# Kernel optimization log

Measured on AMD Instinct MI355X. Metric: run time of the kernel, lower is better.

Reference implementation:

```python
import jax, jax.numpy as jnp
import numpy as np

N_NODES = 50000
IN_DIM = 128
HID = 2 * IN_DIM  # 256, per module: hidden_dim = input_dims * 2
FC1 = 1024
FC2 = 512
N_ACT = 64
N_EDGES = 800000
N_AGENTS = 16384


def _layernorm(h, g, b, eps=1e-5):
    mu = jnp.mean(h, axis=-1, keepdims=True)
    var = jnp.var(h, axis=-1, keepdims=True)
    return (h - mu) * jax.lax.rsqrt(var + eps) * g + b


def setup_inputs() -> dict:
    key = jax.random.key(0)
    ks = jax.random.split(key, 16)
    def u(k, shape, fan_in):
        s = 1.0 / np.sqrt(fan_in)
        return jax.random.uniform(k, shape, jnp.float32, -s, s)
    inp = {}
    inp["x"] = jax.random.normal(ks[0], (N_NODES, IN_DIM), jnp.float32)
    inp["action"] = jax.random.normal(ks[1], (N_AGENTS, N_ACT), jnp.float32)
    inp["edge_index"] = jax.random.randint(ks[2], (2, N_EDGES), 0, N_NODES, jnp.int32)
    inp["agent_idx"] = jax.random.randint(ks[3], (N_AGENTS,), 0, N_NODES, jnp.int32)
    # GCNConv params (linear no bias + separate bias)
    inp["W_gcn"] = u(ks[4], (IN_DIM, HID), IN_DIM)
    inp["b_gcn"] = jnp.zeros((HID,), jnp.float32)
    # fc1, fc2 (custom uniform init per module)
    inp["W1"] = u(ks[5], (HID, FC1), FC1)
    inp["b1"] = u(ks[6], (FC1,), FC1)
    inp["g1"] = jnp.ones((FC1,), jnp.float32)
    inp["beta1"] = jnp.zeros((FC1,), jnp.float32)
    inp["W2"] = u(ks[7], (FC1, FC2), FC2)
    inp["b2"] = u(ks[8], (FC2,), FC2)
    inp["g2"] = jnp.ones((FC2,), jnp.float32)
    inp["beta2"] = jnp.zeros((FC2,), jnp.float32)
    inp["Wa"] = u(ks[9], (N_ACT, FC2), FC2)
    inp["ba"] = u(ks[10], (FC2,), FC2)
    inp["Wq"] = jax.random.uniform(ks[11], (FC2, 1), jnp.float32, -0.003, 0.003)
    inp["bq"] = jax.random.uniform(ks[12], (1,), jnp.float32, -0.003, 0.003)
    return inp


def reference(x, action, W_gcn, b_gcn, W1, b1, g1, beta1, W2, b2, g2, beta2, Wa, ba, Wq, bq, edge_index, agent_idx):
    N = x.shape[0]
    # GCNConv: add self-loops, symmetric D^-1/2 (A+I) D^-1/2 normalization
    loops = jnp.arange(N, dtype=edge_index.dtype)
    src = jnp.concatenate([edge_index[0], loops])
    dst = jnp.concatenate([edge_index[1], loops])
    h = x @ W_gcn  # [N, HID] transform before aggregation
    deg = jax.ops.segment_sum(jnp.ones_like(dst, dtype=h.dtype), dst, num_segments=N)
    dinv = jax.lax.rsqrt(jnp.maximum(deg, 1.0))  # deg >= 1 due to self-loops
    norm = dinv[src] * dinv[dst]  # [E+N]
    agg = jax.ops.segment_sum(h[src] * norm[:, None], dst, num_segments=N) + b_gcn
    # masked gather of agent nodes, then critic MLP
    z = jax.nn.relu(agg[agent_idx])  # [A, HID]
    s = jax.nn.relu(_layernorm(z @ W1 + b1, g1, beta1))
    s = _layernorm(s @ W2 + b2, g2, beta2)
    a = action @ Wa + ba
    sa = jax.nn.relu(s + a)
    return sa @ Wq + bq  # [A, 1]
```

## Files before the change

kernel.cpp:

```cpp
#include <hip/hip_runtime.h>
#include <hip/hip_bf16.h>

typedef _Float16 f16;
typedef _Float16 __attribute__((ext_vector_type(8))) half8;
typedef _Float16 __attribute__((ext_vector_type(4))) half4;
typedef float __attribute__((ext_vector_type(4))) floatx4;

#define IN_DIM 128
#define HID    256
#define FC1    1024
#define FC2    512
#define NACT   64
#define BUCKET 128

__device__ __forceinline__ void transpose_tile(const float* __restrict__ in, f16* __restrict__ out,
                                               int K, int N, int bx, int by, int tid) {
    __shared__ f16 tile[32][33];
    int k0 = bx * 32, n0 = by * 32;
    int tx = tid & 31, ty = tid >> 5;
    #pragma unroll
    for (int i = 0; i < 4; ++i)
        tile[ty + i * 8][tx] = (f16)in[(size_t)(k0 + ty + i * 8) * N + n0 + tx];
    __syncthreads();
    #pragma unroll
    for (int i = 0; i < 4; ++i)
        out[(size_t)(n0 + ty + i * 8) * K + k0 + tx] = tile[tx][ty + i * 8];
}

__device__ __forceinline__ void cvt8(const float* __restrict__ in, f16* __restrict__ out, long gi) {
    float4 a = *(const float4*)&in[gi * 8];
    float4 b = *(const float4*)&in[gi * 8 + 4];
    half8 pk;
    pk[0] = (f16)a.x; pk[1] = (f16)a.y; pk[2] = (f16)a.z; pk[3] = (f16)a.w;
    pk[4] = (f16)b.x; pk[5] = (f16)b.y; pk[6] = (f16)b.z; pk[7] = (f16)b.w;
    *(half8*)&out[gi * 8] = pk;
}

__global__ __launch_bounds__(256)
void prep_kernel(const float* __restrict__ Wgcn, const float* __restrict__ W1,
                 const float* __restrict__ W2, const float* __restrict__ Wa,
                 const float* __restrict__ action, const float* __restrict__ x,
                 f16* WgcnT, f16* W1T, f16* W2T, f16* WaT, f16* act16, f16* x16,
                 int* degcnt, int* needed, int* n_needed, int* cursor, int N, int A) {
    int b = blockIdx.x, tid = threadIdx.x;
    if (b < 196) {
        int i = b * 256 + tid;
        if (i < N) { degcnt[i] = 0; needed[i] = 0; }
        if (b == 0 && tid == 0) *n_needed = 0;
        return;
    }
    b -= 196;
    if (b < 64)  { cursor[b * 256 + tid] = 0; return; }
    b -= 64;
    if (b < 32)  { transpose_tile(Wgcn, WgcnT, IN_DIM, HID, b & 3, b >> 2, tid); return; }
    b -= 32;
    if (b < 256) { transpose_tile(W1, W1T, HID, FC1, b & 7, b >> 3, tid); return; }
    b -= 256;
    if (b < 512) { transpose_tile(W2, W2T, FC1, FC2, b & 31, b >> 5, tid); return; }
    b -= 512;
    if (b < 32)  { transpose_tile(Wa, WaT, NACT, FC2, b & 1, b >> 1, tid); return; }
    b -= 32;
    if (b < 512) { cvt8(action, act16, (long)b * 256 + tid); return; }
    b -= 512;
    cvt8(x, x16, (long)b * 256 + tid);
}

__global__ void markdeg_kernel(const int* __restrict__ agent_idx, const int* __restrict__ edst,
                               int* __restrict__ needed, int* __restrict__ needed_list,
                               int* __restrict__ n_needed, int* __restrict__ degcnt, int A, int E) {
    int b = blockIdx.x;
    if (b < 64) {
        int i = b * 256 + threadIdx.x;
        if (i < A) {
            int idx = agent_idx[i];
            if (atomicCAS(&needed[idx], 0, -1) == 0) {
                int p = atomicAdd(n_needed, 1);
                needed_list[p] = idx;
                needed[idx] = p + 1;
            }
        }
        return;
    }
    int e = (b - 64) * 256 + threadIdx.x;
    if (e < E) atomicAdd(&degcnt[edst[e]], 1);
}

__global__ void dssfill_kernel(const int* __restrict__ degcnt, const int* __restrict__ needed,
                               const int* __restrict__ agent_idx, float* __restrict__ dinv,
                               int* __restrict__ agent_slot,
                               const int* __restrict__ esrc, const int* __restrict__ edst,
                               int* __restrict__ cursor, int* __restrict__ srcbuf,
                               int N, int A, int E) {
    int b = blockIdx.x;
    int tid = threadIdx.x;
    if (b < 196) {
        int i = b * 256 + tid;
        if (i < N) dinv[i] = rsqrtf((float)degcnt[i] + 1.0f);
        return;
    }
    b -= 196;
    if (b < 64) {
        int i = b * 256 + tid;
        if (i < A) agent_slot[i] = needed[agent_idx[i]] - 1;
        return;
    }
    b -= 64;
    int e = b * 256 + tid;
    if (e < E) {
        int d = edst[e];
        int s = needed[d];
        if (s != 0) {
            int slot = s - 1;
            int pos = atomicAdd(&cursor[slot], 1);
            if (pos < BUCKET) srcbuf[slot * BUCKET + pos] = esrc[e];
        }
    }
}

__global__ __launch_bounds__(256)
void gather_x_kernel(const int* __restrict__ needed_list, const int* __restrict__ n_needed,
                     const int* __restrict__ degcnt,
                     const int* __restrict__ srcbuf, const float* __restrict__ dinv,
                     const f16* __restrict__ x16, f16* __restrict__ xagg) {
    int w = (blockIdx.x * 256 + threadIdx.x) >> 6;
    int lane = threadIdx.x & 63;
    if (w >= *n_needed) return;
    int d = needed_list[w];
    float dd = dinv[d];
    int beg = w * BUCKET;
    int cnt = degcnt[d];
    if (cnt > BUCKET) cnt = BUCKET;
    union { unsigned u; f16 h[2]; } ld0, ld1, ld2, ld3;
    ld0.u = *(const unsigned*)&x16[(size_t)d * IN_DIM + lane * 2];
    float ax = (float)ld0.h[0] * dd * dd, ay = (float)ld0.h[1] * dd * dd;
    int j = 0;
    for (; j + 3 < cnt; j += 4) {
        int s0 = srcbuf[beg + j], s1 = srcbuf[beg + j + 1];
        int s2 = srcbuf[beg + j + 2], s3 = srcbuf[beg + j + 3];
        float n0 = dinv[s0] * dd, n1 = dinv[s1] * dd;
        float n2 = dinv[s2] * dd, n3 = dinv[s3] * dd;
        ld0.u = *(const unsigned*)&x16[(size_t)s0 * IN_DIM + lane * 2];
        ld1.u = *(const unsigned*)&x16[(size_t)s1 * IN_DIM + lane * 2];
        ld2.u = *(const unsigned*)&x16[(size_t)s2 * IN_DIM + lane * 2];
        ld3.u = *(const unsigned*)&x16[(size_t)s3 * IN_DIM + lane * 2];
        ax = fmaf((float)ld0.h[0], n0, ax); ay = fmaf((float)ld0.h[1], n0, ay);
        ax = fmaf((float)ld1.h[0], n1, ax); ay = fmaf((float)ld1.h[1], n1, ay);
        ax = fmaf((float)ld2.h[0], n2, ax); ay = fmaf((float)ld2.h[1], n2, ay);
        ax = fmaf((float)ld3.h[0], n3, ax); ay = fmaf((float)ld3.h[1], n3, ay);
    }
    for (; j < cnt; ++j) {
        int s0 = srcbuf[beg + j];
        float n0 = dinv[s0] * dd;
        ld0.u = *(const unsigned*)&x16[(size_t)s0 * IN_DIM + lane * 2];
        ax = fmaf((float)ld0.h[0], n0, ax);
        ay = fmaf((float)ld0.h[1], n0, ay);
    }
    union { f16 h[2]; unsigned u; } pk;
    pk.h[0] = (f16)ax; pk.h[1] = (f16)ay;
    *(unsigned*)&xagg[(size_t)w * IN_DIM + lane * 2] = pk.u;
}

__device__ __forceinline__ void swz_decode(int bid, int log2ny, int& bx, int& by) {
    int xcd = bid & 7;
    int pos = bid >> 3;
    bx = (pos >> log2ny) * 8 + xcd;
    by = pos & ((1 << log2ny) - 1);
}

template<bool RELU, bool LIMIT>
__device__ __forceinline__ void gemm_tile64(f16* __restrict__ smA, f16* __restrict__ smB,
                                            const f16* __restrict__ A, const f16* __restrict__ BT,
                                            f16* __restrict__ C, const float* __restrict__ bias,
                                            const int* __restrict__ limit,
                                            int bx, int by, int N, int K) {
    if (LIMIT && bx * 64 >= *limit) return;
    const int tid = threadIdx.x;
    const int lane = tid & 63;
    const int wave = tid >> 6;
    const int wr = wave >> 1, wc = wave & 1;
    const long bm = (long)bx * 64, bn = (long)by * 64;

    size_t aoff[2], boff[2];
    #pragma unroll
    for (int t = 0; t < 2; ++t) {
        int ci = t * 256 + tid;
        int r = ci >> 3, s = ci & 7, ks = s ^ (r & 7);
        aoff[t] = (size_t)(bm + r) * K + ks * 8;
        boff[t] = (size_t)(bn + r) * K + ks * 8;
    }
    int aidx[2][2], bidx[2][2];
    const int kc = lane >> 4;
    #pragma unroll
    for (int kk = 0; kk < 2; ++kk) {
        #pragma unroll
        for (int i = 0; i < 2; ++i) {
            int ar = wr * 32 + i * 16 + (lane & 15);
            aidx[kk][i] = ar * 64 + ((kk * 4 + kc) ^ (ar & 7)) * 8;
            int br = wc * 32 + i * 16 + (lane & 15);
            bidx[kk][i] = br * 64 + ((kk * 4 + kc) ^ (br & 7)) * 8;
        }
    }

    const int NT = K >> 6;
    auto stage = [&](int buf, int k0) {
        #pragma unroll
        for (int t = 0; t < 2; ++t) {
            __builtin_amdgcn_global_load_lds(
                (const __attribute__((address_space(1))) void*)(A + aoff[t] + k0),
                (__attribute__((address_space(3))) void*)(&smA[buf * 4096 + (t * 256 + tid) * 8]), 16, 0, 0);
            __builtin_amdgcn_global_load_lds(
                (const __attribute__((address_space(1))) void*)(BT + boff[t] + k0),
                (__attribute__((address_space(3))) void*)(&smB[buf * 4096 + (t * 256 + tid) * 8]), 16, 0, 0);
        }
    };

    floatx4 acc[2][2] = {};
    stage(0, 0);
    asm volatile("s_waitcnt vmcnt(0)" ::: "memory");
    __builtin_amdgcn_s_barrier();
    int cur = 0;
    for (int t = 0; t < NT; ++t) {
        if (t + 1 < NT) stage(cur ^ 1, (t + 1) << 6);
        #pragma unroll
        for (int kk = 0; kk < 2; ++kk) {
            half8 af[2], bf[2];
            #pragma unroll
            for (int i = 0; i < 2; ++i) {
                af[i] = *(const half8*)&smA[cur * 4096 + aidx[kk][i]];
                bf[i] = *(const half8*)&smB[cur * 4096 + bidx[kk][i]];
            }
            #pragma unroll
            for (int mi = 0; mi < 2; ++mi)
                #pragma unroll
                for (int ni = 0; ni < 2; ++ni)
                    acc[mi][ni] = __builtin_amdgcn_mfma_f32_16x16x32_f16(af[mi], bf[ni], acc[mi][ni], 0, 0, 0);
        }
        asm volatile("s_waitcnt vmcnt(0)" ::: "memory");
        __builtin_amdgcn_s_barrier();
        cur ^= 1;
    }
    const int col0 = (int)bn + wc * 32 + (lane & 15);
    const int row0 = (int)bm + wr * 32 + (lane >> 4) * 4;
    #pragma unroll
    for (int ni = 0; ni < 2; ++ni) {
        int col = col0 + ni * 16;
        float bz = bias[col];
        #pragma unroll
        for (int mi = 0; mi < 2; ++mi) {
            #pragma unroll
            for (int q = 0; q < 4; ++q) {
                int row = row0 + mi * 16 + q;
                float v = acc[mi][ni][q] + bz;
                if (RELU) v = fmaxf(v, 0.f);
                C[(size_t)row * N + col] = (f16)v;
            }
        }
    }
}

template<bool RELU, bool LIMIT>
__global__ __launch_bounds__(256)
void gemm64_kernel(const f16* __restrict__ A, const f16* __restrict__ BT,
                   f16* __restrict__ C, const float* __restrict__ bias,
                   const int* __restrict__ limit, int N, int K, int log2ny) {
    __shared__ __align__(16) f16 smA[2 * 4096];
    __shared__ __align__(16) f16 smB[2 * 4096];
    int bx, by;
    swz_decode(blockIdx.x, log2ny, bx, by);
    gemm_tile64<RELU, LIMIT>(smA, smB, A, BT, C, bias, limit, bx, by, N, K);
}

template<bool LIMIT>
__device__ __forceinline__ void gemm_tile128(f16* __restrict__ smA, f16* __restrict__ smB,
                                             const f16* __restrict__ A, const f16* __restrict__ BT,
                                             f16* __restrict__ C, const float* __restrict__ bias,
                                             const int* __restrict__ limit,
                                             int bx, int by, int N, int K) {
    if (LIMIT && bx * 128 >= *limit) return;
    const int tid = threadIdx.x;
    const int lane = tid & 63;
    const int wave = tid >> 6;
    const int wr = wave >> 1, wc = wave & 1;
    const long bm = (long)bx * 128, bn = (long)by * 128;

    size_t aoff[4], boff[4];
    #pragma unroll
    for (int t = 0; t < 4; ++t) {
        int ci = t * 256 + tid;
        int r = ci >> 3, s = ci & 7, ks = s ^ (r & 7);
        aoff[t] = (size_t)(bm + r) * K + ks * 8;
        boff[t] = (size_t)(bn + r) * K + ks * 8;
    }
    int aidx[2][4], bidx[2][4];
    const int kc = lane >> 4;
    #pragma unroll
    for (int kk = 0; kk < 2; ++kk) {
        #pragma unroll
        for (int i = 0; i < 4; ++i) {
            int ar = wr * 64 + i * 16 + (lane & 15);
            aidx[kk][i] = ar * 64 + ((kk * 4 + kc) ^ (ar & 7)) * 8;
            int br = wc * 64 + i * 16 + (lane & 15);
            bidx[kk][i] = br * 64 + ((kk * 4 + kc) ^ (br & 7)) * 8;
        }
    }

    const int NT = K >> 6;
    auto stage = [&](int buf, int k0) {
        #pragma unroll
        for (int t = 0; t < 4; ++t) {
            __builtin_amdgcn_global_load_lds(
                (const __attribute__((address_space(1))) void*)(A + aoff[t] + k0),
                (__attribute__((address_space(3))) void*)(&smA[buf * 8192 + (t * 256 + tid) * 8]), 16, 0, 0);
            __builtin_amdgcn_global_load_lds(
                (const __attribute__((address_space(1))) void*)(BT + boff[t] + k0),
                (__attribute__((address_space(3))) void*)(&smB[buf * 8192 + (t * 256 + tid) * 8]), 16, 0, 0);
        }
    };

    floatx4 acc[4][4] = {};
    stage(0, 0);
    asm volatile("s_waitcnt vmcnt(0)" ::: "memory");
    __builtin_amdgcn_s_barrier();
    int cur = 0;
    for (int t = 0; t < NT; ++t) {
        if (t + 1 < NT) stage(cur ^ 1, (t + 1) << 6);
        #pragma unroll
        for (int kk = 0; kk < 2; ++kk) {
            half8 af[4], bf[4];
            #pragma unroll
            for (int i = 0; i < 4; ++i) {
                af[i] = *(const half8*)&smA[cur * 8192 + aidx[kk][i]];
                bf[i] = *(const half8*)&smB[cur * 8192 + bidx[kk][i]];
            }
            #pragma unroll
            for (int mi = 0; mi < 4; ++mi)
                #pragma unroll
                for (int ni = 0; ni < 4; ++ni)
                    acc[mi][ni] = __builtin_amdgcn_mfma_f32_16x16x32_f16(af[mi], bf[ni], acc[mi][ni], 0, 0, 0);
        }
        asm volatile("s_waitcnt vmcnt(0)" ::: "memory");
        __builtin_amdgcn_s_barrier();
        cur ^= 1;
    }
    const int col0 = (int)bn + wc * 64 + (lane & 15);
    const int row0 = (int)bm + wr * 64 + (lane >> 4) * 4;
    #pragma unroll
    for (int ni = 0; ni < 4; ++ni) {
        int col = col0 + ni * 16;
        float bz = bias[col];
        #pragma unroll
        for (int mi = 0; mi < 4; ++mi) {
            #pragma unroll
            for (int q = 0; q < 4; ++q) {
                int row = row0 + mi * 16 + q;
                C[(size_t)row * N + col] = (f16)(acc[mi][ni][q] + bz);
            }
        }
    }
}

template<bool LIMIT>
__global__ __launch_bounds__(256)
void gemm128_kernel(const f16* __restrict__ A, const f16* __restrict__ BT,
                    f16* __restrict__ C, const float* __restrict__ bias,
                    const int* __restrict__ limit, int N, int K, int log2ny) {
    __shared__ __align__(16) f16 smA[2 * 8192];
    __shared__ __align__(16) f16 smB[2 * 8192];
    int bx, by;
    swz_decode(blockIdx.x, log2ny, bx, by);
    gemm_tile128<LIMIT>(smA, smB, A, BT, C, bias, limit, bx, by, N, K);
}

__global__ __launch_bounds__(256)
void gemm_dual_kernel(const f16* __restrict__ A0, const f16* __restrict__ BT0, f16* __restrict__ C0,
                      const float* __restrict__ bias0, const int* __restrict__ limit, int K0,
                      const f16* __restrict__ A1, const f16* __restrict__ BT1, f16* __restrict__ C1,
                      const float* __restrict__ bias1, int K1, int half, int N) {
    __shared__ __align__(16) f16 smA[2 * 8192];
    __shared__ __align__(16) f16 smB[2 * 8192];
    int bid = blockIdx.x;
    int bx, by;
    if (bid < half) {
        swz_decode(bid, 2, bx, by);
        gemm_tile128<true>(smA, smB, A0, BT0, C0, bias0, limit, bx, by, N, K0);
    } else {
        swz_decode(bid - half, 2, bx, by);
        gemm_tile128<false>(smA, smB, A1, BT1, C1, bias1, nullptr, bx, by, N, K1);
    }
}

__global__ __launch_bounds__(256)
void ln_relu_f16_kernel(f16* __restrict__ s, const float* __restrict__ g,
                        const float* __restrict__ b, const int* __restrict__ nn) {
    int row = blockIdx.x;
    if (row >= *nn) return;
    f16* p = s + (size_t)row * FC1;
    int tid = threadIdx.x;
    half4 v = *(const half4*)&p[tid * 4];
    float f0 = (float)v[0], f1 = (float)v[1], f2 = (float)v[2], f3 = (float)v[3];
    float sum = f0 + f1 + f2 + f3;
    float sq = f0 * f0 + f1 * f1 + f2 * f2 + f3 * f3;
    #pragma unroll
    for (int off = 32; off > 0; off >>= 1) {
        sum += __shfl_down(sum, off);
        sq  += __shfl_down(sq, off);
    }
    __shared__ float ssum[4], ssq[4];
    int wid = tid >> 6;
    if ((tid & 63) == 0) { ssum[wid] = sum; ssq[wid] = sq; }
    __syncthreads();
    float tot = ssum[0] + ssum[1] + ssum[2] + ssum[3];
    float tq  = ssq[0] + ssq[1] + ssq[2] + ssq[3];
    float mu = tot * (1.0f / FC1);
    float var = tq * (1.0f / FC1) - mu * mu;
    float rs = rsqrtf(var + 1e-5f);
    float4 gg = *(const float4*)&g[tid * 4];
    float4 bb = *(const float4*)&b[tid * 4];
    half4 o;
    o[0] = (f16)fmaxf((f0 - mu) * rs * gg.x + bb.x, 0.f);
    o[1] = (f16)fmaxf((f1 - mu) * rs * gg.y + bb.y, 0.f);
    o[2] = (f16)fmaxf((f2 - mu) * rs * gg.z + bb.z, 0.f);
    o[3] = (f16)fmaxf((f3 - mu) * rs * gg.w + bb.w, 0.f);
    *(half4*)&p[tid * 4] = o;
}

__global__ __launch_bounds__(256)
void final_f16_kernel(const f16* __restrict__ s2, const f16* __restrict__ ab,
                      const int* __restrict__ agent_slot,
                      const float* __restrict__ g2, const float* __restrict__ b2,
                      const float* __restrict__ Wq, const float* __restrict__ bq,
                      float* __restrict__ out) {
    int row = blockIdx.x;
    int slot = agent_slot[row];
    const f16* p = s2 + (size_t)slot * FC2;
    int tid = threadIdx.x;
    float v0 = (float)p[tid * 2], v1 = (float)p[tid * 2 + 1];
    float sum = v0 + v1;
    float sq = v0 * v0 + v1 * v1;
    #pragma unroll
    for (int off = 32; off > 0; off >>= 1) {
        sum += __shfl_down(sum, off);
        sq  += __shfl_down(sq, off);
    }
    __shared__ float ssum[4], ssq[4], spart[4];
    int wid = tid >> 6;
    if ((tid & 63) == 0) { ssum[wid] = sum; ssq[wid] = sq; }
    __syncthreads();
    float tot = ssum[0] + ssum[1] + ssum[2] + ssum[3];
    float tq  = ssq[0] + ssq[1] + ssq[2] + ssq[3];
    float mu = tot * (1.0f / FC2);
    float var = tq * (1.0f / FC2) - mu * mu;
    float rs = rsqrtf(var + 1e-5f);
    float a0 = (float)ab[(size_t)row * FC2 + tid * 2];
    float a1 = (float)ab[(size_t)row * FC2 + tid * 2 + 1];
    float g0 = g2[tid * 2], g1 = g2[tid * 2 + 1];
    float bb0 = b2[tid * 2], bb1 = b2[tid * 2 + 1];
    float sa0 = fmaxf((v0 - mu) * rs * g0 + bb0 + a0, 0.f);
    float sa1 = fmaxf((v1 - mu) * rs * g1 + bb1 + a1, 0.f);
    float part = sa0 * Wq[tid * 2] + sa1 * Wq[tid * 2 + 1];
    #pragma unroll
    for (int off = 32; off > 0; off >>= 1) part += __shfl_down(part, off);
    if ((tid & 63) == 0) spart[wid] = part;
    __syncthreads();
    if (tid == 0) out[row] = spart[0] + spart[1] + spart[2] + spart[3] + bq[0];
}

extern "C" void kernel_launch(void* const* d_in, const int* in_sizes, int n_in,
                              void* d_out, int out_size, void* d_ws, size_t ws_size,
                              hipStream_t stream) {
    const float* x        = (const float*)d_in[0];
    const float* action   = (const float*)d_in[1];
    const int*   edge     = (const int*)d_in[2];
    const int*   agent_idx= (const int*)d_in[3];
    const float* W_gcn    = (const float*)d_in[4];
    const float* b_gcn    = (const float*)d_in[5];
    const float* W1       = (const float*)d_in[6];
    const float* b1       = (const float*)d_in[7];
    const float* g1       = (const float*)d_in[8];
    const float* beta1    = (const float*)d_in[9];
    const float* W2       = (const float*)d_in[10];
    const float* b2       = (const float*)d_in[11];
    const float* g2       = (const float*)d_in[12];
    const float* beta2    = (const float*)d_in[13];
    const float* Wa       = (const float*)d_in[14];
    const float* ba       = (const float*)d_in[15];
    const float* Wq       = (const float*)d_in[16];
    const float* bq       = (const float*)d_in[17];
    float* out = (float*)d_out;

    const int N = in_sizes[0] / IN_DIM;
    const int E = in_sizes[2] / 2;
    const int A = in_sizes[3];
    const int* esrc = edge;
    const int* edst = edge + E;

    char* ws = (char*)d_ws;
    size_t off = 0;
    auto carve = [&](size_t bytes) -> char* {
        char* p = ws + off;
        off += (bytes + 255) & ~(size_t)255;
        return p;
    };
    int*   degcnt     = (int*)  carve((size_t)N * 4);
    int*   needed     = (int*)  carve((size_t)N * 4);
    float* dinv       = (float*)carve((size_t)N * 4);
    int*   cursor     = (int*)  carve((size_t)A * 4);
    int*   needed_list= (int*)  carve((size_t)A * 4);
    int*   n_needed   = (int*)  carve(256);
    int*   agent_slot = (int*)  carve((size_t)A * 4);
    int*   srcbuf     = (int*)  carve((size_t)A * BUCKET * 4);
    f16*   WgcnT      = (f16*)  carve((size_t)HID * IN_DIM * 2);
    f16*   W1T        = (f16*)  carve((size_t)FC1 * HID * 2);
    f16*   W2T        = (f16*)  carve((size_t)FC2 * FC1 * 2);
    f16*   WaT        = (f16*)  carve((size_t)FC2 * NACT * 2);
    f16*   act16      = (f16*)  carve((size_t)A * NACT * 2);
    f16*   x16        = (f16*)  carve((size_t)N * IN_DIM * 2);
    f16*   xagg       = (f16*)  carve((size_t)A * IN_DIM * 2);
    f16*   z          = (f16*)  carve((size_t)A * HID * 2);
    f16*   s1         = (f16*)  carve((size_t)A * FC1 * 2);
    f16*   s2         = (f16*)  carve((size_t)A * FC2 * 2);
    f16*   abuf       = (f16*)  carve((size_t)A * FC2 * 2);
    (void)ws_size;

    const int eblk = (E + 255) / 256;

    prep_kernel<<<196 + 64 + 32 + 256 + 512 + 32 + 512 + eblk, 256, 0, stream>>>(
        W_gcn, W1, W2, Wa, action, x, WgcnT, W1T, W2T, WaT, act16, x16,
        degcnt, needed, n_needed, cursor, N, A);
    markdeg_kernel<<<64 + eblk, 256, 0, stream>>>(agent_idx, edst, needed, needed_list,
                                                  n_needed, degcnt, A, E);
    dssfill_kernel<<<196 + 64 + eblk, 256, 0, stream>>>(degcnt, needed, agent_idx, dinv,
                                                        agent_slot, esrc, edst, cursor,
                                                        srcbuf, N, A, E);
    gather_x_kernel<<<(A + 3) / 4, 256, 0, stream>>>(needed_list, n_needed, degcnt,
                                                     srcbuf, dinv, x16, xagg);
    gemm64_kernel<true, true><<<(A / 64) * (HID / 64), 256, 0, stream>>>(
        xagg, WgcnT, z, b_gcn, n_needed, HID, IN_DIM, 2);
    gemm128_kernel<true><<<(A / 128) * (FC1 / 128), 256, 0, stream>>>(
        z, W1T, s1, b1, n_needed, FC1, HID, 3);
    ln_relu_f16_kernel<<<A, 256, 0, stream>>>(s1, g1, beta1, n_needed);
    gemm_dual_kernel<<<2 * (A / 128) * (FC2 / 128), 256, 0, stream>>>(
        s1, W2T, s2, b2, n_needed, FC1,
        act16, WaT, abuf, ba, NACT, (A / 128) * (FC2 / 128), FC2);
    final_f16_kernel<<<A, 256, 0, stream>>>(s2, abuf, agent_slot, g2, beta2, Wq, bq, out);
}
```

Before: 158.5 us.

## Merge degree count and edge bucketing into one kernel keyed by node

Folds the degree-count and source-bucketing kernels into a single build kernel, removing one launch and the dependency on the needed-slot lookup. Edges are now bucketed for every destination node rather than only needed ones, and dinv/agent_slot arrays are dropped in favour of computing rsqrt from degcnt inline in the gather and looking up slots in the final kernel. This trades a launch and a dinv pass for bucketing all edges, so it adds atomic and scattered-write traffic into a much larger srcbuf. It also looks like a race: the same grid's bucketing blocks may run while degree atomics are still in progress. The gather itself reads only degcnt after the kernel finishes, so results stay correct.

```diff
diff --git a/kernel.cpp b/kernel.cpp
--- a/kernel.cpp
+++ b/kernel.cpp
@@ -50,8 +50,8 @@
         return;
     }
     b -= 196;
-    if (b < 64)  { cursor[b * 256 + tid] = 0; return; }
-    b -= 64;
+    if (b < 196) { int i = b * 256 + tid; if (i < N) cursor[i] = 0; return; }
+    b -= 196;
     if (b < 32)  { transpose_tile(Wgcn, WgcnT, IN_DIM, HID, b & 3, b >> 2, tid); return; }
     b -= 32;
     if (b < 256) { transpose_tile(W1, W1T, HID, FC1, b & 7, b >> 3, tid); return; }
@@ -65,12 +65,16 @@
     cvt8(x, x16, (long)b * 256 + tid);
 }
 
-__global__ void markdeg_kernel(const int* __restrict__ agent_idx, const int* __restrict__ edst,
-                               int* __restrict__ needed, int* __restrict__ needed_list,
-                               int* __restrict__ n_needed, int* __restrict__ degcnt, int A, int E) {
+__global__ void build_kernel(const int* __restrict__ agent_idx,
+                             const int* __restrict__ esrc, const int* __restrict__ edst,
+                             int* __restrict__ needed, int* __restrict__ needed_list,
+                             int* __restrict__ n_needed, int* __restrict__ degcnt,
+                             int* __restrict__ cursor, int* __restrict__ srcbuf,
+                             int A, int E, int eblk) {
     int b = blockIdx.x;
+    int tid = threadIdx.x;
     if (b < 64) {
-        int i = b * 256 + threadIdx.x;
+        int i = b * 256 + tid;
         if (i < A) {
             int idx = agent_idx[i];
             if (atomicCAS(&needed[idx], 0, -1) == 0) {
@@ -81,53 +85,31 @@
         }
         return;
     }
-    int e = (b - 64) * 256 + threadIdx.x;
-    if (e < E) atomicAdd(&degcnt[edst[e]], 1);
-}
-
-__global__ void dssfill_kernel(const int* __restrict__ degcnt, const int* __restrict__ needed,
-                               const int* __restrict__ agent_idx, float* __restrict__ dinv,
-                               int* __restrict__ agent_slot,
-                               const int* __restrict__ esrc, const int* __restrict__ edst,
-                               int* __restrict__ cursor, int* __restrict__ srcbuf,
-                               int N, int A, int E) {
-    int b = blockIdx.x;
-    int tid = threadIdx.x;
-    if (b < 196) {
-        int i = b * 256 + tid;
-        if (i < N) dinv[i] = rsqrtf((float)degcnt[i] + 1.0f);
+    b -= 64;
+    if (b < eblk) {
+        int e = b * 256 + tid;
+        if (e < E) atomicAdd(&degcnt[edst[e]], 1);
         return;
     }
-    b -= 196;
-    if (b < 64) {
-        int i = b * 256 + tid;
-        if (i < A) agent_slot[i] = needed[agent_idx[i]] - 1;
-        return;
-    }
-    b -= 64;
+    b -= eblk;
     int e = b * 256 + tid;
     if (e < E) {
         int d = edst[e];
-        int s = needed[d];
-        if (s != 0) {
-            int slot = s - 1;
-            int pos = atomicAdd(&cursor[slot], 1);
-            if (pos < BUCKET) srcbuf[slot * BUCKET + pos] = esrc[e];
-        }
+        int pos = atomicAdd(&cursor[d], 1);
+        if (pos < BUCKET) srcbuf[(size_t)d * BUCKET + pos] = esrc[e];
     }
 }
 
 __global__ __launch_bounds__(256)
 void gather_x_kernel(const int* __restrict__ needed_list, const int* __restrict__ n_needed,
-                     const int* __restrict__ degcnt,
-                     const int* __restrict__ srcbuf, const float* __restrict__ dinv,
+                     const int* __restrict__ degcnt, const int* __restrict__ srcbuf,
                      const f16* __restrict__ x16, f16* __restrict__ xagg) {
     int w = (blockIdx.x * 256 + threadIdx.x) >> 6;
     int lane = threadIdx.x & 63;
     if (w >= *n_needed) return;
     int d = needed_list[w];
-    float dd = dinv[d];
-    int beg = w * BUCKET;
+    float dd = rsqrtf((float)degcnt[d] + 1.0f);
+    size_t beg = (size_t)d * BUCKET;
     int cnt = degcnt[d];
     if (cnt > BUCKET) cnt = BUCKET;
     union { unsigned u; f16 h[2]; } ld0, ld1, ld2, ld3;
@@ -137,8 +119,10 @@
     for (; j + 3 < cnt; j += 4) {
         int s0 = srcbuf[beg + j], s1 = srcbuf[beg + j + 1];
         int s2 = srcbuf[beg + j + 2], s3 = srcbuf[beg + j + 3];
-        float n0 = dinv[s0] * dd, n1 = dinv[s1] * dd;
-        float n2 = dinv[s2] * dd, n3 = dinv[s3] * dd;
+        float n0 = rsqrtf((float)degcnt[s0] + 1.0f) * dd;
+        float n1 = rsqrtf((float)degcnt[s1] + 1.0f) * dd;
+        float n2 = rsqrtf((float)degcnt[s2] + 1.0f) * dd;
+        float n3 = rsqrtf((float)degcnt[s3] + 1.0f) * dd;
         ld0.u = *(const unsigned*)&x16[(size_t)s0 * IN_DIM + lane * 2];
         ld1.u = *(const unsigned*)&x16[(size_t)s1 * IN_DIM + lane * 2];
         ld2.u = *(const unsigned*)&x16[(size_t)s2 * IN_DIM + lane * 2];
@@ -150,7 +134,7 @@
     }
     for (; j < cnt; ++j) {
         int s0 = srcbuf[beg + j];
-        float n0 = dinv[s0] * dd;
+        float n0 = rsqrtf((float)degcnt[s0] + 1.0f) * dd;
         ld0.u = *(const unsigned*)&x16[(size_t)s0 * IN_DIM + lane * 2];
         ax = fmaf((float)ld0.h[0], n0, ax);
         ay = fmaf((float)ld0.h[1], n0, ay);
@@ -426,12 +410,12 @@
 
 __global__ __launch_bounds__(256)
 void final_f16_kernel(const f16* __restrict__ s2, const f16* __restrict__ ab,
-                      const int* __restrict__ agent_slot,
+                      const int* __restrict__ agent_idx, const int* __restrict__ needed,
                       const float* __restrict__ g2, const float* __restrict__ b2,
                       const float* __restrict__ Wq, const float* __restrict__ bq,
                       float* __restrict__ out) {
     int row = blockIdx.x;
-    int slot = agent_slot[row];
+    int slot = needed[agent_idx[row]] - 1;
     const f16* p = s2 + (size_t)slot * FC2;
     int tid = threadIdx.x;
     float v0 = (float)p[tid * 2], v1 = (float)p[tid * 2 + 1];
@@ -503,12 +487,10 @@
     };
     int*   degcnt     = (int*)  carve((size_t)N * 4);
     int*   needed     = (int*)  carve((size_t)N * 4);
-    float* dinv       = (float*)carve((size_t)N * 4);
-    int*   cursor     = (int*)  carve((size_t)A * 4);
+    int*   cursor     = (int*)  carve((size_t)N * 4);
     int*   needed_list= (int*)  carve((size_t)A * 4);
     int*   n_needed   = (int*)  carve(256);
-    int*   agent_slot = (int*)  carve((size_t)A * 4);
-    int*   srcbuf     = (int*)  carve((size_t)A * BUCKET * 4);
+    int*   srcbuf     = (int*)  carve((size_t)N * BUCKET * 4);
     f16*   WgcnT      = (f16*)  carve((size_t)HID * IN_DIM * 2);
     f16*   W1T        = (f16*)  carve((size_t)FC1 * HID * 2);
     f16*   W2T        = (f16*)  carve((size_t)FC2 * FC1 * 2);
@@ -524,16 +506,14 @@
 
     const int eblk = (E + 255) / 256;
 
-    prep_kernel<<<196 + 64 + 32 + 256 + 512 + 32 + 512 + eblk, 256, 0, stream>>>(
+    prep_kernel<<<196 + 196 + 32 + 256 + 512 + 32 + 512 + eblk, 256, 0, stream>>>(
         W_gcn, W1, W2, Wa, action, x, WgcnT, W1T, W2T, WaT, act16, x16,
         degcnt, needed, n_needed, cursor, N, A);
-    markdeg_kernel<<<64 + eblk, 256, 0, stream>>>(agent_idx, edst, needed, needed_list,
-                                                  n_needed, degcnt, A, E);
-    dssfill_kernel<<<196 + 64 + eblk, 256, 0, stream>>>(degcnt, needed, agent_idx, dinv,
-                                                        agent_slot, esrc, edst, cursor,
-                                                        srcbuf, N, A, E);
+    build_kernel<<<64 + 2 * eblk, 256, 0, stream>>>(agent_idx, esrc, edst, needed,
+                                                    needed_list, n_needed, degcnt,
+                                                    cursor, srcbuf, A, E, eblk);
     gather_x_kernel<<<(A + 3) / 4, 256, 0, stream>>>(needed_list, n_needed, degcnt,
-                                                     srcbuf, dinv, x16, xagg);
+                                                     srcbuf, x16, xagg);
     gemm64_kernel<true, true><<<(A / 64) * (HID / 64), 256, 0, stream>>>(
         xagg, WgcnT, z, b_gcn, n_needed, HID, IN_DIM, 2);
     gemm128_kernel<true><<<(A / 128) * (FC1 / 128), 256, 0, stream>>>(
@@ -542,5 +522,5 @@
     gemm_dual_kernel<<<2 * (A / 128) * (FC2 / 128), 256, 0, stream>>>(
         s1, W2T, s2, b2, n_needed, FC1,
         act16, WaT, abuf, ba, NACT, (A / 128) * (FC2 / 128), FC2);
-    final_f16_kernel<<<A, 256, 0, stream>>>(s2, abuf, agent_slot, g2, beta2, Wq, bq, out);
-}
+    final_f16_kernel<<<A, 256, 0, stream>>>(s2, abuf, agent_idx, needed, g2, beta2, Wq, bq, out);
+}
```

New measurement: 187.6 us. 18.3% more time.
